# Optimization experiments

Hardware: AMD Instinct MI355X
Metric: run time of the kernel (lower is better)

Reference implementation:

```python
import jax, jax.numpy as jnp
import numpy as np

ALPHA = 0.1  # dt/tau = 10/100


def setup_inputs() -> dict:
    key = jax.random.key(0)
    k1, k2, k3 = jax.random.split(key, 3)
    seq_len, batch, in_dim, hid = 1024, 64, 128, 512
    inp = jax.random.normal(k1, (seq_len, batch, in_dim), dtype=jnp.float32)
    W_in = jax.random.normal(k2, (hid, in_dim), dtype=jnp.float32) / np.sqrt(in_dim)
    b_in = jnp.zeros((hid,), dtype=jnp.float32)
    W_hid = jax.random.normal(k3, (hid, hid), dtype=jnp.float32) / np.sqrt(hid)
    b_hid = jnp.zeros((hid,), dtype=jnp.float32)
    return {"input": inp, "W_in": W_in, "b_in": b_in, "W_hid": W_hid, "b_hid": b_hid}


def reference(input, W_in, b_in, W_hid, b_hid):
    # leaky RNN: v_t = (1-a) v_{t-1} + a (W_hid fr_{t-1} + b_hid + W_in u_t + b_in)
    #            fr_t = relu(v_t)
    hid = W_hid.shape[0]
    batch = input.shape[1]
    # precompute input projection for all steps: (seq, batch, hid)
    u_proj = jnp.einsum('sbi,hi->sbh', input, W_in) + b_in

    v0 = jnp.zeros((batch, hid), dtype=input.dtype)
    fr0 = jax.nn.relu(v0)

    def step(carry, u_t):
        fr, v = carry
        v = (1.0 - ALPHA) * v + ALPHA * (fr @ W_hid.T + b_hid + u_t)
        fr = jax.nn.relu(v)
        return (fr, v), fr

    _, states = jax.lax.scan(step, (fr0, v0), u_proj)
    return states  # (seq_len, batch, hidden)
```

## Files before the change

### kernel.cpp

```cpp
#include <hip/hip_runtime.h>
#include <hip/hip_bf16.h>
#include <stdint.h>


#define SEQ   1024
#define BATCH 64
#define INDIM 128
#define HID   512
#define HG    16
#define BGN   4
#define SXS   20

typedef __attribute__((ext_vector_type(8))) short   short8;
typedef __attribute__((ext_vector_type(4))) float   floatx4;
typedef unsigned long long ull;

__device__ __forceinline__ unsigned short f2bf(float x) {
  union { float f; unsigned int u; } v; v.f = x;
  unsigned int r = v.u + 0x7fffu + ((v.u >> 16) & 1u);
  return (unsigned short)(r >> 16);
}
__device__ __forceinline__ ull pack4(unsigned short a, unsigned short b,
                                     unsigned short c, unsigned short d) {
  return (ull)a | ((ull)b << 16) | ((ull)c << 32) | ((ull)d << 48);
}

#define TA_SB 64
#define TA_H  128
#define TA_K  64
#define APAD  65

__global__ __launch_bounds__(256) void uproj_kernel(
    const float* __restrict__ inp, const float* __restrict__ Win,
    const float* __restrict__ bin, float* __restrict__ out)
{
  __shared__ float sIn[TA_SB * APAD];
  __shared__ float sW [TA_H  * APAD];
  const int tid = threadIdx.x;
  const int sb0 = (blockIdx.x >> 2) * TA_SB;
  const int h0  = (blockIdx.x & 3) * TA_H;
  const int tx = tid & 15, ty = tid >> 4;

  float acc[4][8];
  #pragma unroll
  for (int i = 0; i < 4; ++i)
    #pragma unroll
    for (int j = 0; j < 8; ++j) acc[i][j] = 0.f;

  for (int kt = 0; kt < INDIM / TA_K; ++kt) {
    #pragma unroll
    for (int p = 0; p < 4; ++p) {
      int idx = tid + 256 * p;
      int row = idx >> 4, c4 = (idx & 15) << 2;
      const float4 v = *(const float4*)(inp + (size_t)(sb0 + row) * INDIM + kt * TA_K + c4);
      float* d = sIn + row * APAD + c4;
      d[0] = v.x; d[1] = v.y; d[2] = v.z; d[3] = v.w;
    }
    #pragma unroll
    for (int p = 0; p < 8; ++p) {
      int idx = tid + 256 * p;
      int row = idx >> 4, c4 = (idx & 15) << 2;
      const float4 v = *(const float4*)(Win + (size_t)(h0 + row) * INDIM + kt * TA_K + c4);
      float* d = sW + row * APAD + c4;
      d[0] = v.x; d[1] = v.y; d[2] = v.z; d[3] = v.w;
    }
    __syncthreads();

    for (int k = 0; k < TA_K; ++k) {
      float a[4], b[8];
      #pragma unroll
      for (int i = 0; i < 4; ++i) a[i] = sIn[(ty + 16 * i) * APAD + k];
      #pragma unroll
      for (int j = 0; j < 8; ++j) b[j] = sW[(tx + 16 * j) * APAD + k];
      #pragma unroll
      for (int i = 0; i < 4; ++i)
        #pragma unroll
        for (int j = 0; j < 8; ++j) acc[i][j] = fmaf(a[i], b[j], acc[i][j]);
    }
    __syncthreads();
  }

  #pragma unroll
  for (int j = 0; j < 8; ++j) {
    float bb = bin[h0 + tx + 16 * j];
    #pragma unroll
    for (int i = 0; i < 4; ++i)
      out[(size_t)(sb0 + ty + 16 * i) * HID + h0 + tx + 16 * j] = acc[i][j] + bb;
  }
}

__global__ __launch_bounds__(128) void scan_kernel(
    const float* __restrict__ Whid, const float* __restrict__ bhid,
    float* __restrict__ uo,
    ull* __restrict__ frA)
{
  __shared__ unsigned short sX[32 * SXS];

  const int tid  = threadIdx.x;
  const int lane = tid & 63;
  const int wave = tid >> 6;
  const int bg = blockIdx.x >> 4;
  const int hg = blockIdx.x & 15;
  const int b0 = bg * 16;
  const int h0 = hg * 32;

  const int cn = lane & 15;
  const int q  = lane >> 4;
  const int mq = q * 4;
  const int nl = wave * 16 + cn;
  const int ng = h0 + nl;
  const float bias = bhid[ng];

  short8 bw[HG];
  {
    const float* wrow = Whid + (size_t)ng * HID + q * 8;
    #pragma unroll
    for (int kk = 0; kk < HG; ++kk) {
      const float4 a = *(const float4*)(wrow + kk * 32);
      const float4 b = *(const float4*)(wrow + kk * 32 + 4);
      union { unsigned short s[8]; short8 v; } u;
      u.s[0] = f2bf(a.x); u.s[1] = f2bf(a.y); u.s[2] = f2bf(a.z); u.s[3] = f2bf(a.w);
      u.s[4] = f2bf(b.x); u.s[5] = f2bf(b.y); u.s[6] = f2bf(b.z); u.s[7] = f2bf(b.w);
      bw[kk] = u.v;
    }
  }

  const int pl  = tid >> 1, ph = tid & 1;
  const int pm  = pl & 15;
  const int pk0 = (pl >> 4) * 8 + ph * 4;

  const ull MASKT = 0x8000800080008000ull;
  float v[4] = {0.f, 0.f, 0.f, 0.f};
  const float OMA = 0.9f, AL = 0.1f;

  for (int t = 0; t < SEQ; ++t) {
    const float* up = uo + ((size_t)t * BATCH + b0 + mq) * HID + ng;
    float uu[4];
    #pragma unroll
    for (int r = 0; r < 4; ++r) uu[r] = up[(size_t)r * HID];

    floatx4 acc[4];
    #pragma unroll
    for (int j = 0; j < 4; ++j) acc[j] = (floatx4){0.f, 0.f, 0.f, 0.f};

    if (t > 0) {
      const int slot = (t - 1) & 1;
      const ull expv = (((t - 1) >> 1) & 1) ? MASKT : 0ull;
      const ull* ap = frA + (size_t)(slot * BGN + bg) * HG * 128 + (size_t)lane * 2;
      ull lo[HG], hi[HG];
      for (;;) {
        int ok = 1;
        #pragma unroll
        for (int kk = 0; kk < HG; ++kk) {
          lo[kk] = __hip_atomic_load(ap + (size_t)kk * 128,
                                     __ATOMIC_RELAXED, __HIP_MEMORY_SCOPE_AGENT);
          hi[kk] = __hip_atomic_load(ap + (size_t)kk * 128 + 1,
                                     __ATOMIC_RELAXED, __HIP_MEMORY_SCOPE_AGENT);
          ok &= (int)(((lo[kk] & MASKT) == expv) & ((hi[kk] & MASKT) == expv));
        }
        if (__all(ok)) break;
      }
      #pragma unroll
      for (int kk = 0; kk < HG; ++kk) {
        union { ull u[2]; short8 s; } af;
        af.u[0] = lo[kk] & ~MASKT;
        af.u[1] = hi[kk] & ~MASKT;
        acc[kk & 3] = __builtin_amdgcn_mfma_f32_16x16x32_bf16(af.s, bw[kk],
                                                              acc[kk & 3], 0, 0, 0);
      }
    }

    float fr[4];
    #pragma unroll
    for (int r = 0; r < 4; ++r) {
      float s = acc[0][r] + acc[1][r] + acc[2][r] + acc[3][r];
      v[r] = OMA * v[r] + AL * (s + bias + uu[r]);
      fr[r] = fmaxf(v[r], 0.f);
    }

    *(ull*)(sX + nl * SXS + mq) = pack4(f2bf(fr[0]), f2bf(fr[1]),
                                        f2bf(fr[2]), f2bf(fr[3]));
    __syncthreads();
    {
      unsigned short g0 = sX[(pk0 + 0) * SXS + pm];
      unsigned short g1 = sX[(pk0 + 1) * SXS + pm];
      unsigned short g2 = sX[(pk0 + 2) * SXS + pm];
      unsigned short g3 = sX[(pk0 + 3) * SXS + pm];
      ull pk = pack4(g0, g1, g2, g3);
      if ((t >> 1) & 1) pk |= MASKT;
      ull* dst = frA + (size_t)(((t & 1) * BGN + bg) * HG + hg) * 128
                     + (size_t)pl * 2 + ph;
      __hip_atomic_store(dst, pk, __ATOMIC_RELAXED, __HIP_MEMORY_SCOPE_AGENT);
    }

    float* op = uo + ((size_t)t * BATCH + b0 + mq) * HID + ng;
    #pragma unroll
    for (int r = 0; r < 4; ++r) op[(size_t)r * HID] = fr[r];

    __syncthreads();
  }
}

extern "C" void kernel_launch(void* const* d_in, const int* in_sizes, int n_in,
                              void* d_out, int out_size, void* d_ws, size_t ws_size,
                              hipStream_t stream) {
  const float* inp  = (const float*)d_in[0];
  const float* Win  = (const float*)d_in[1];
  const float* bin  = (const float*)d_in[2];
  const float* Whid = (const float*)d_in[3];
  const float* bhid = (const float*)d_in[4];
  float* out = (float*)d_out;

  ull* frA = (ull*)d_ws;

  uproj_kernel<<<dim3((65536 / TA_SB) * (HID / TA_H)), dim3(256), 0, stream>>>(
      inp, Win, bin, out);
  scan_kernel<<<dim3(BGN * HG), dim3(128), 0, stream>>>(
      Whid, bhid, out, frA);
}
```

Measured before the change: 2.414 ms.

## Swap MFMA operands so each lane owns contiguous hidden units, drop LDS transpose

The MFMA operands are swapped (weights as A, activations as B), so each lane's accumulator holds four consecutive hidden units for one batch row. That lets each lane pack and publish its bf16 outputs directly, removing the shared-memory transpose and both per-step __syncthreads. The u-projection load and the output store become single float4 accesses, and the bias is loaded as a float4. The atomic loads and stores are also widened to system scope, which may add coherence cost to the spin-wait loop.

```diff
diff --git a/kernel.cpp b/kernel.cpp
--- a/kernel.cpp
+++ b/kernel.cpp
@@ -9,7 +9,6 @@
 #define HID   512
 #define HG    16
 #define BGN   4
-#define SXS   20
 
 typedef __attribute__((ext_vector_type(8))) short   short8;
 typedef __attribute__((ext_vector_type(4))) float   floatx4;
@@ -94,8 +93,6 @@
     float* __restrict__ uo,
     ull* __restrict__ frA)
 {
-  __shared__ unsigned short sX[32 * SXS];
-
   const int tid  = threadIdx.x;
   const int lane = tid & 63;
   const int wave = tid >> 6;
@@ -104,16 +101,14 @@
   const int b0 = bg * 16;
   const int h0 = hg * 32;
 
-  const int cn = lane & 15;
-  const int q  = lane >> 4;
-  const int mq = q * 4;
-  const int nl = wave * 16 + cn;
-  const int ng = h0 + nl;
-  const float bias = bhid[ng];
-
-  short8 bw[HG];
+  const int m   = lane & 15;
+  const int q   = lane >> 4;
+  const int nb  = wave * 16 + q * 4;
+  const int ng  = h0 + nb;
+
+  short8 ww[HG];
   {
-    const float* wrow = Whid + (size_t)ng * HID + q * 8;
+    const float* wrow = Whid + (size_t)(h0 + wave * 16 + m) * HID + q * 8;
     #pragma unroll
     for (int kk = 0; kk < HG; ++kk) {
       const float4 a = *(const float4*)(wrow + kk * 32);
@@ -121,23 +116,22 @@
       union { unsigned short s[8]; short8 v; } u;
       u.s[0] = f2bf(a.x); u.s[1] = f2bf(a.y); u.s[2] = f2bf(a.z); u.s[3] = f2bf(a.w);
       u.s[4] = f2bf(b.x); u.s[5] = f2bf(b.y); u.s[6] = f2bf(b.z); u.s[7] = f2bf(b.w);
-      bw[kk] = u.v;
-    }
-  }
-
-  const int pl  = tid >> 1, ph = tid & 1;
-  const int pm  = pl & 15;
-  const int pk0 = (pl >> 4) * 8 + ph * 4;
+      ww[kk] = u.v;
+    }
+  }
+
+  const float4 bias = *(const float4*)(bhid + ng);
+
+  ull* const pub = frA;
+  const int pml  = m + 16 * ((nb >> 3) & 3);
+  const int phh  = (nb >> 2) & 1;
 
   const ull MASKT = 0x8000800080008000ull;
-  float v[4] = {0.f, 0.f, 0.f, 0.f};
+  floatx4 v = {0.f, 0.f, 0.f, 0.f};
   const float OMA = 0.9f, AL = 0.1f;
 
   for (int t = 0; t < SEQ; ++t) {
-    const float* up = uo + ((size_t)t * BATCH + b0 + mq) * HID + ng;
-    float uu[4];
-    #pragma unroll
-    for (int r = 0; r < 4; ++r) uu[r] = up[(size_t)r * HID];
+    const float4 uu = *(const float4*)(uo + ((size_t)t * BATCH + b0 + m) * HID + ng);
 
     floatx4 acc[4];
     #pragma unroll
@@ -153,9 +147,9 @@
         #pragma unroll
         for (int kk = 0; kk < HG; ++kk) {
           lo[kk] = __hip_atomic_load(ap + (size_t)kk * 128,
-                                     __ATOMIC_RELAXED, __HIP_MEMORY_SCOPE_AGENT);
+                                     __ATOMIC_RELAXED, __HIP_MEMORY_SCOPE_SYSTEM);
           hi[kk] = __hip_atomic_load(ap + (size_t)kk * 128 + 1,
-                                     __ATOMIC_RELAXED, __HIP_MEMORY_SCOPE_AGENT);
+                                     __ATOMIC_RELAXED, __HIP_MEMORY_SCOPE_SYSTEM);
           ok &= (int)(((lo[kk] & MASKT) == expv) & ((hi[kk] & MASKT) == expv));
         }
         if (__all(ok)) break;
@@ -165,39 +159,36 @@
         union { ull u[2]; short8 s; } af;
         af.u[0] = lo[kk] & ~MASKT;
         af.u[1] = hi[kk] & ~MASKT;
-        acc[kk & 3] = __builtin_amdgcn_mfma_f32_16x16x32_bf16(af.s, bw[kk],
+        acc[kk & 3] = __builtin_amdgcn_mfma_f32_16x16x32_bf16(ww[kk], af.s,
                                                               acc[kk & 3], 0, 0, 0);
       }
     }
 
     float fr[4];
-    #pragma unroll
-    for (int r = 0; r < 4; ++r) {
-      float s = acc[0][r] + acc[1][r] + acc[2][r] + acc[3][r];
-      v[r] = OMA * v[r] + AL * (s + bias + uu[r]);
-      fr[r] = fmaxf(v[r], 0.f);
-    }
-
-    *(ull*)(sX + nl * SXS + mq) = pack4(f2bf(fr[0]), f2bf(fr[1]),
-                                        f2bf(fr[2]), f2bf(fr[3]));
-    __syncthreads();
+    fr[0] = 0.f; fr[1] = 0.f; fr[2] = 0.f; fr[3] = 0.f;
     {
-      unsigned short g0 = sX[(pk0 + 0) * SXS + pm];
-      unsigned short g1 = sX[(pk0 + 1) * SXS + pm];
-      unsigned short g2 = sX[(pk0 + 2) * SXS + pm];
-      unsigned short g3 = sX[(pk0 + 3) * SXS + pm];
-      ull pk = pack4(g0, g1, g2, g3);
+      const float ub[4] = {uu.x, uu.y, uu.z, uu.w};
+      const float bb[4] = {bias.x, bias.y, bias.z, bias.w};
+      #pragma unroll
+      for (int r = 0; r < 4; ++r) {
+        float s = acc[0][r] + acc[1][r] + acc[2][r] + acc[3][r];
+        v[r] = OMA * v[r] + AL * (s + bb[r] + ub[r]);
+        fr[r] = fmaxf(v[r], 0.f);
+      }
+    }
+
+    {
+      ull pk = pack4(f2bf(fr[0]), f2bf(fr[1]), f2bf(fr[2]), f2bf(fr[3]));
       if ((t >> 1) & 1) pk |= MASKT;
-      ull* dst = frA + (size_t)(((t & 1) * BGN + bg) * HG + hg) * 128
-                     + (size_t)pl * 2 + ph;
-      __hip_atomic_store(dst, pk, __ATOMIC_RELAXED, __HIP_MEMORY_SCOPE_AGENT);
-    }
-
-    float* op = uo + ((size_t)t * BATCH + b0 + mq) * HID + ng;
-    #pragma unroll
-    for (int r = 0; r < 4; ++r) op[(size_t)r * HID] = fr[r];
-
-    __syncthreads();
+      ull* dst = pub + (size_t)(((t & 1) * BGN + bg) * HG + hg) * 128
+                     + (size_t)pml * 2 + phh;
+      __hip_atomic_store(dst, pk, __ATOMIC_RELAXED, __HIP_MEMORY_SCOPE_SYSTEM);
+    }
+
+    {
+      float4 o; o.x = fr[0]; o.y = fr[1]; o.z = fr[2]; o.w = fr[3];
+      *(float4*)(uo + ((size_t)t * BATCH + b0 + m) * HID + ng) = o;
+    }
   }
 }
 
```

Result: slower. 2.640 ms (+9.4%).
